# Kernel tuning notes

Measured on AMD Instinct MI355X. Metric: run time of the kernel, lower is better.

Reference implementation:

```python
import jax, jax.numpy as jnp
import numpy as np

B, DIM, H, W = 2, 128, 64, 64
DH, HEADS, K = 32, 4, 7  # dim_head, num_heads = dim // dim_head, kernel_size


def _ln(x, g, b):
    mu = jnp.mean(x, -1, keepdims=True)
    var = jnp.mean((x - mu) ** 2, -1, keepdims=True)
    return (x - mu) * jax.lax.rsqrt(var + 1e-5) * g + b


def _na2d(x, qkv_w, qkv_b, rpb, proj_w, proj_b):
    # NATTEN-style 2D neighborhood attention, dilation=1, edge-clamped windows.
    Bb, Hh, Ww, C = x.shape
    k = K
    qkv = (x @ qkv_w.T + qkv_b).reshape(Bb, Hh, Ww, 3, HEADS, DH).transpose(3, 0, 4, 1, 2, 5)
    q = qkv[0] * (DH ** -0.5)  # [B, heads, H, W, dh]
    kt, vt = qkv[1], qkv[2]
    def starts(n):
        return jnp.clip(jnp.arange(n) - k // 2, 0, n - k)
    nh = starts(Hh)[:, None] + jnp.arange(k)  # [H, k] absolute neighbor rows
    nw = starts(Ww)[:, None] + jnp.arange(k)  # [W, k] absolute neighbor cols
    ih = nh[:, None, :, None]  # [H,1,k,1]
    iw = nw[None, :, None, :]  # [1,W,1,k]
    Kw = kt[:, :, ih, iw, :]   # [B, heads, H, W, k, k, dh]
    Vw = vt[:, :, ih, iw, :]
    attn = jnp.einsum('bnhwd,bnhwijd->bnhwij', q, Kw)  # [B,heads,H,W,k,k]
    # relative positional bias, indices in [0, 2k-2]
    bih = (nh - jnp.arange(Hh)[:, None] + (k - 1))[:, None, :, None]
    biw = (nw - jnp.arange(Ww)[:, None] + (k - 1))[None, :, None, :]
    attn = attn + rpb[:, bih, biw][None]
    attn = jax.nn.softmax(attn.reshape(Bb, HEADS, Hh, Ww, k * k), -1).reshape(Bb, HEADS, Hh, Ww, k, k)
    out = jnp.einsum('bnhwij,bnhwijd->bnhwd', attn, Vw)
    out = out.transpose(0, 2, 3, 1, 4).reshape(Bb, Hh, Ww, C)
    return out @ proj_w.T + proj_b


def setup_inputs() -> dict:
    key = jax.random.key(0)
    ks = jax.random.split(key, 8)
    d = DIM
    w = lambda k_, sh: jax.random.normal(k_, sh, jnp.float32) * 0.02
    inp = {'x': jax.random.normal(ks[0], (B, DIM, H, W), jnp.float32)}
    inp.update(g1=jnp.ones(d), be1=jnp.zeros(d), g2=jnp.ones(d), be2=jnp.zeros(d),
               g3=jnp.ones(d), be3=jnp.zeros(d), g4=jnp.ones(d), be4=jnp.zeros(d))
    inp['qkv_w'] = w(ks[1], (3 * d, d)); inp['qkv_b'] = jnp.zeros(3 * d)
    inp['rpb'] = w(ks[2], (HEADS, 2 * K - 1, 2 * K - 1))
    inp['proj_w'] = w(ks[3], (d, d)); inp['proj_b'] = jnp.zeros(d)
    inp['w1'] = w(ks[4], (d, d)); inp['bl1'] = jnp.zeros(d)
    inp['w2'] = w(ks[5], (d, d)); inp['bl2'] = jnp.zeros(d)
    inp['w3'] = w(ks[6], (d, d)); inp['bl3'] = jnp.zeros(d)
    return inp


def reference(x, g1, be1, g2, be2, g3, be3, g4, be4, qkv_w, qkv_b, rpb, proj_w, proj_b, w1, bl1, w2, bl2, w3, bl3):
    x = x.transpose(0, 2, 3, 1)  # NCHW -> NHWC
    r = x
    y = _ln(x, g1, be1)
    y = _na2d(y, qkv_w, qkv_b, rpb, proj_w, proj_b)
    y = _ln(y, g2, be2)
    y = y @ w1.T + bl1
    x = y + r
    r = x
    y = _ln(x, g3, be3)
    y = y @ w2.T + bl2
    y = jax.nn.relu(y)
    y = _ln(y, g4, be4)
    y = y @ w3.T + bl3
    x = y + r
    return x.transpose(0, 3, 1, 2)  # NHWC -> NCHW
```

## Files before the change

### kernel.cpp

```cpp
#include <hip/hip_runtime.h>
#include <hip/hip_bf16.h>
#include <cstdint>

typedef short bf16x8 __attribute__((ext_vector_type(8)));
typedef float f32x4 __attribute__((ext_vector_type(4)));

#define NTOK 8192
#define QSCALE 0.17677669529663687f

__device__ inline float b2f(short s) {
  return __uint_as_float(((unsigned)(unsigned short)s) << 16);
}
__device__ inline short f2bs(float x) {
  __hip_bfloat16 b = __float2bfloat16(x);
  return *reinterpret_cast<short*>(&b);
}
__device__ inline bf16x8 ld8(const short* p) {
  short4 lo = *reinterpret_cast<const short4*>(p);
  short4 hi = *reinterpret_cast<const short4*>(p + 4);
  bf16x8 r;
  r[0] = lo.x; r[1] = lo.y; r[2] = lo.z; r[3] = lo.w;
  r[4] = hi.x; r[5] = hi.y; r[6] = hi.z; r[7] = hi.w;
  return r;
}
__device__ inline bf16x8 cvt8(float4 a, float4 c) {
  bf16x8 r;
  r[0] = f2bs(a.x); r[1] = f2bs(a.y); r[2] = f2bs(a.z); r[3] = f2bs(a.w);
  r[4] = f2bs(c.x); r[5] = f2bs(c.y); r[6] = f2bs(c.z); r[7] = f2bs(c.w);
  return r;
}

__global__ __launch_bounds__(512) void k_qkvcw(
    const float* __restrict__ x, const float* __restrict__ g,
    const float* __restrict__ be, const float* __restrict__ qkv_b,
    const float* __restrict__ qkv_w, const float* __restrict__ pw,
    const float* __restrict__ w1f, const float* __restrict__ w2f,
    const float* __restrict__ w3f, __hip_bfloat16* __restrict__ wb,
    float* __restrict__ r, __hip_bfloat16* __restrict__ qkvb) {
  __shared__ float xt[128][33];
  __shared__ __hip_bfloat16 at[32][136];
  int t = threadIdx.x;
  if (t < 256) {
    int ci = blockIdx.x * 256 + t;
    float cv;
    if (ci < 16384) cv = pw[ci];
    else if (ci < 32768) cv = w1f[ci - 16384];
    else if (ci < 49152) cv = w2f[ci - 32768];
    else cv = w3f[ci - 49152];
    wb[ci] = __float2bfloat16(cv);
  }
  int m0 = blockIdx.x * 32;
  int b = m0 >> 12;
  int p0 = m0 & 4095;
  const float* xb = x + (size_t)b * 524288;
  int tw = t & 31, th = t >> 5;
#pragma unroll
  for (int i = 0; i < 8; ++i) {
    int c = i * 16 + th;
    xt[c][tw] = xb[c * 4096 + p0 + tw];
  }
  __syncthreads();
  int wid = t >> 6, lane = t & 63;
  float gg0 = g[lane], gg1 = g[lane + 64];
  float bb0 = be[lane], bb1 = be[lane + 64];
#pragma unroll
  for (int it = 0; it < 4; ++it) {
    int tt = wid * 4 + it;
    float v0 = xt[lane][tt], v1 = xt[lane + 64][tt];
    float s = v0 + v1, sq = v0 * v0 + v1 * v1;
#pragma unroll
    for (int off = 32; off; off >>= 1) {
      s += __shfl_xor(s, off);
      sq += __shfl_xor(sq, off);
    }
    float mu = s * (1.f / 128.f);
    float var = sq * (1.f / 128.f) - mu * mu;
    float rs = rsqrtf(var + 1e-5f);
    r[(size_t)(m0 + tt) * 128 + lane] = v0;
    r[(size_t)(m0 + tt) * 128 + 64 + lane] = v1;
    at[tt][lane] = __float2bfloat16((v0 - mu) * rs * gg0 + bb0);
    at[tt][lane + 64] = __float2bfloat16((v1 - mu) * rs * gg1 + bb1);
  }
  __syncthreads();
  int mw = wid >> 2, nwq = wid & 3;
  int lr = lane & 15, kg = lane >> 4;
  bf16x8 af[4];
#pragma unroll
  for (int ks = 0; ks < 4; ++ks)
    af[ks] = *reinterpret_cast<const bf16x8*>(&at[mw * 16 + lr][ks * 32 + kg * 8]);
  f32x4 acc[6];
#pragma unroll
  for (int nf = 0; nf < 6; ++nf) acc[nf] = f32x4{0, 0, 0, 0};
#pragma unroll
  for (int nf = 0; nf < 6; ++nf) {
    int o = nwq * 96 + nf * 16 + lr;
    const float* wp = qkv_w + o * 128 + kg * 8;
#pragma unroll
    for (int ks = 0; ks < 4; ++ks) {
      float4 wa = *reinterpret_cast<const float4*>(wp + ks * 32);
      float4 wc = *reinterpret_cast<const float4*>(wp + ks * 32 + 4);
      acc[nf] = __builtin_amdgcn_mfma_f32_16x16x32_bf16(af[ks], cvt8(wa, wc),
                                                        acc[nf], 0, 0, 0);
    }
  }
#pragma unroll
  for (int nf = 0; nf < 6; ++nf) {
    int o = nwq * 96 + nf * 16 + lr;
    float bv = qkv_b[o];
    float qs = (o < 128) ? QSCALE : 1.f;
#pragma unroll
    for (int rr = 0; rr < 4; ++rr) {
      int m = m0 + mw * 16 + kg * 4 + rr;
      qkvb[(size_t)m * 384 + o] = __float2bfloat16((acc[nf][rr] + bv) * qs);
    }
  }
}

#define NB 98
#define VP 108
#define VPD 54
#define PP 132
__global__ __launch_bounds__(256) void k_attn4(
    const __hip_bfloat16* __restrict__ qkv, const float* __restrict__ rpb,
    __hip_bfloat16* __restrict__ ao) {
  __shared__ __align__(16) short smem[128 * VP + 4 * 8 * PP];
  short* Vt = smem;
  short* Pl = smem + 128 * VP;
  const short* qs = (const short*)qkv;
  int tid = threadIdx.x;
  int bid = blockIdx.x;
  int swz = (bid & 7) * 128 + (bid >> 3);
  int m0 = swz * 8;
  int b = m0 >> 12, hq = (m0 >> 6) & 63, c0 = m0 & 63;
  int hs = min(max(hq - 3, 0), 57);
  int cs0 = min(max(c0 - 3, 0), 50);
  unsigned* VtD = (unsigned*)Vt;
  {
    int g2 = tid >> 6, rp = tid & 63;
    if (rp < 49) {
      int r0 = rp * 2, r1 = r0 + 1;
      int rh0 = r0 / 14, rc0 = r0 - rh0 * 14;
      int rh1 = r1 / 14, rc1 = r1 - rh1 * 14;
      int tr0 = b * 4096 + (hs + rh0) * 64 + min(cs0 + rc0, 63);
      int tr1 = b * 4096 + (hs + rh1) * 64 + min(cs0 + rc1, 63);
#pragma unroll
      for (int gg = 0; gg < 4; ++gg) {
        int d0 = (g2 * 4 + gg) * 8;
        const short* p0 = qs + (size_t)tr0 * 384 + 256 + d0;
        const short* p1 = qs + (size_t)tr1 * 384 + 256 + d0;
        short4 a0 = *(const short4*)p0, a1 = *(const short4*)(p0 + 4);
        short4 c0v = *(const short4*)p1, c1 = *(const short4*)(p1 + 4);
        unsigned bse = (unsigned)d0 * VPD + rp;
        VtD[bse + 0 * VPD] = (unsigned short)a0.x | ((unsigned)(unsigned short)c0v.x << 16);
        VtD[bse + 1 * VPD] = (unsigned short)a0.y | ((unsigned)(unsigned short)c0v.y << 16);
        VtD[bse + 2 * VPD] = (unsigned short)a0.z | ((unsigned)(unsigned short)c0v.z << 16);
        VtD[bse + 3 * VPD] = (unsigned short)a0.w | ((unsigned)(unsigned short)c0v.w << 16);
        VtD[bse + 4 * VPD] = (unsigned short)a1.x | ((unsigned)(unsigned short)c1.x << 16);
        VtD[bse + 5 * VPD] = (unsigned short)a1.y | ((unsigned)(unsigned short)c1.y << 16);
        VtD[bse + 6 * VPD] = (unsigned short)a1.z | ((unsigned)(unsigned short)c1.z << 16);
        VtD[bse + 7 * VPD] = (unsigned short)a1.w | ((unsigned)(unsigned short)c1.w << 16);
      }
    }
  }
  for (int i = tid; i < 128 * 5; i += 256) {
    int d = i / 5, j = i - d * 5;
    VtD[d * VPD + 49 + j] = 0;
  }
  int h = tid >> 6, lane = tid & 63;
  int lr = lane & 15, kg = lane >> 4;
  int qrow = min(m0 + lr, NTOK - 1);
  bf16x8 aq = *reinterpret_cast<const bf16x8*>(qs + (size_t)qrow * 384 + h * 32 + kg * 8);
  f32x4 sc[7];
#pragma unroll
  for (int nt = 0; nt < 7; ++nt) {
    int nbr = nt * 16 + lr;
    int rw = min(nbr, NB - 1);
    int rh = rw / 14, rc = rw - rh * 14;
    int tn = b * 4096 + (hs + rh) * 64 + min(cs0 + rc, 63);
    bf16x8 bk = *reinterpret_cast<const bf16x8*>(qs + (size_t)tn * 384 + 128 + h * 32 + kg * 8);
    sc[nt] = __builtin_amdgcn_mfma_f32_16x16x32_bf16(aq, bk, f32x4{0, 0, 0, 0}, 0, 0, 0);
  }
  int offv[4], cmt[4];
#pragma unroll
  for (int rr = 0; rr < 4; ++rr) {
    int ct = c0 + kg * 4 + rr;
    int ws0 = min(max(ct - 3, 0), 57);
    offv[rr] = ws0 - cs0;
    cmt[rr] = cs0 + 6 - ct;
  }
  float mx[4] = {-3e38f, -3e38f, -3e38f, -3e38f};
#pragma unroll
  for (int nt = 0; nt < 7; ++nt) {
    int nbr = nt * 16 + lr;
    int rh = nbr / 14, rc = nbr - rh * 14;
    bool vn = nbr < NB;
    int ribase = h * 169 + (hs - hq + 6 + rh) * 13 + rc;
#pragma unroll
    for (int rr = 0; rr < 4; ++rr) {
      float v = -1e30f;
      if (vn && (unsigned)(rc - offv[rr]) < 7u) v = sc[nt][rr] + rpb[ribase + cmt[rr]];
      sc[nt][rr] = v;
      mx[rr] = fmaxf(mx[rr], v);
    }
  }
#pragma unroll
  for (int rr = 0; rr < 4; ++rr) {
    mx[rr] = fmaxf(mx[rr], __shfl_xor(mx[rr], 1));
    mx[rr] = fmaxf(mx[rr], __shfl_xor(mx[rr], 2));
    mx[rr] = fmaxf(mx[rr], __shfl_xor(mx[rr], 4));
    mx[rr] = fmaxf(mx[rr], __shfl_xor(mx[rr], 8));
  }
  float sum[4] = {0.f, 0.f, 0.f, 0.f};
#pragma unroll
  for (int nt = 0; nt < 7; ++nt)
#pragma unroll
    for (int rr = 0; rr < 4; ++rr) {
      float e = __expf(sc[nt][rr] - mx[rr]);
      sc[nt][rr] = e;
      sum[rr] += e;
    }
#pragma unroll
  for (int rr = 0; rr < 4; ++rr) {
    sum[rr] += __shfl_xor(sum[rr], 1);
    sum[rr] += __shfl_xor(sum[rr], 2);
    sum[rr] += __shfl_xor(sum[rr], 4);
    sum[rr] += __shfl_xor(sum[rr], 8);
  }
  short* Ph = Pl + h * 8 * PP;
  if (kg < 2) {
#pragma unroll
    for (int rr = 0; rr < 4; ++rr) {
      float inv = 1.f / sum[rr];
      int tok = kg * 4 + rr;
#pragma unroll
      for (int nt = 0; nt < 7; ++nt)
        Ph[tok * PP + nt * 16 + lr] = f2bs(sc[nt][rr] * inv);
      Ph[tok * PP + 112 + lr] = 0;
      Ph[tok * PP + 128 + (lr & 3)] = 0;
    }
  }
  __syncthreads();
  f32x4 o[2] = {f32x4{0, 0, 0, 0}, f32x4{0, 0, 0, 0}};
#pragma unroll
  for (int kt = 0; kt < 4; ++kt) {
    bf16x8 ap = ld8(Ph + (lr & 7) * PP + kt * 32 + kg * 8);
#pragma unroll
    for (int dt = 0; dt < 2; ++dt) {
      bf16x8 bv = ld8(Vt + (h * 32 + dt * 16 + lr) * VP + kt * 32 + kg * 8);
      o[dt] = __builtin_amdgcn_mfma_f32_16x16x32_bf16(ap, bv, o[dt], 0, 0, 0);
    }
  }
  if (kg < 2) {
#pragma unroll
    for (int dt = 0; dt < 2; ++dt)
#pragma unroll
      for (int rr = 0; rr < 4; ++rr) {
        int tok = kg * 4 + rr;
        ao[(size_t)(m0 + tok) * 128 + h * 32 + dt * 16 + lr] =
            __float2bfloat16(o[dt][rr]);
      }
  }
}

__global__ __launch_bounds__(512) void k_tail(
    const __hip_bfloat16* __restrict__ ao, const float* __restrict__ r,
    const __hip_bfloat16* __restrict__ wb, const float* __restrict__ bproj,
    const float* __restrict__ g2, const float* __restrict__ be2,
    const float* __restrict__ b1,
    const float* __restrict__ g3, const float* __restrict__ be3,
    const float* __restrict__ b2,
    const float* __restrict__ g4, const float* __restrict__ be4,
    const float* __restrict__ b3, float* __restrict__ out) {
  __shared__ __hip_bfloat16 abuf[32][136];
  __shared__ float2 red[2][4][16];
  int t = threadIdx.x, wid = t >> 6, lane = t & 63;
  int mw = wid >> 2, nwq = wid & 3;
  int lr = lane & 15, kg = lane >> 4;
  int m0 = blockIdx.x * 32;
  const __hip_bfloat16* wproj = wb;
  const __hip_bfloat16* w1 = wb + 16384;
  const __hip_bfloat16* w2 = wb + 32768;
  const __hip_bfloat16* w3 = wb + 49152;
  f32x4 acc[2];
  float x2f[2][4];

  auto gemm_glob = [&](const __hip_bfloat16* Aglob, const __hip_bfloat16* W) {
    bf16x8 af[4];
#pragma unroll
    for (int ks = 0; ks < 4; ++ks)
      af[ks] = *reinterpret_cast<const bf16x8*>(Aglob + (mw * 16 + lr) * 128 + ks * 32 + kg * 8);
#pragma unroll
    for (int nf = 0; nf < 2; ++nf) {
      int o = nwq * 32 + nf * 16 + lr;
      const __hip_bfloat16* wp = W + o * 128 + kg * 8;
      acc[nf] = f32x4{0, 0, 0, 0};
#pragma unroll
      for (int ks = 0; ks < 4; ++ks) {
        bf16x8 bfr = *reinterpret_cast<const bf16x8*>(wp + ks * 32);
        acc[nf] = __builtin_amdgcn_mfma_f32_16x16x32_bf16(af[ks], bfr, acc[nf], 0, 0, 0);
      }
    }
  };
  auto gemm_lds = [&](const __hip_bfloat16* W) {
    bf16x8 af[4];
#pragma unroll
    for (int ks = 0; ks < 4; ++ks)
      af[ks] = *reinterpret_cast<const bf16x8*>(&abuf[mw * 16 + lr][ks * 32 + kg * 8]);
#pragma unroll
    for (int nf = 0; nf < 2; ++nf) {
      int o = nwq * 32 + nf * 16 + lr;
      const __hip_bfloat16* wp = W + o * 128 + kg * 8;
      acc[nf] = f32x4{0, 0, 0, 0};
#pragma unroll
      for (int ks = 0; ks < 4; ++ks) {
        bf16x8 bfr = *reinterpret_cast<const bf16x8*>(wp + ks * 32);
        acc[nf] = __builtin_amdgcn_mfma_f32_16x16x32_bf16(af[ks], bfr, acc[nf], 0, 0, 0);
      }
    }
  };
  auto ln_store = [&](const float* g, const float* be) {
    float ps[4] = {0.f, 0.f, 0.f, 0.f}, pq[4] = {0.f, 0.f, 0.f, 0.f};
#pragma unroll
    for (int nf = 0; nf < 2; ++nf)
#pragma unroll
      for (int rr = 0; rr < 4; ++rr) {
        float v = acc[nf][rr];
        ps[rr] += v;
        pq[rr] += v * v;
      }
#pragma unroll
    for (int rr = 0; rr < 4; ++rr)
#pragma unroll
      for (int off = 1; off < 16; off <<= 1) {
        ps[rr] += __shfl_xor(ps[rr], off);
        pq[rr] += __shfl_xor(pq[rr], off);
      }
    if (lr == 0)
#pragma unroll
      for (int rr = 0; rr < 4; ++rr)
        red[mw][nwq][kg * 4 + rr] = make_float2(ps[rr], pq[rr]);
    __syncthreads();
    float mu[4], rs[4];
#pragma unroll
    for (int rr = 0; rr < 4; ++rr) {
      int r16 = kg * 4 + rr;
      float2 a0 = red[mw][0][r16], a1 = red[mw][1][r16];
      float2 a2 = red[mw][2][r16], a3 = red[mw][3][r16];
      float ssum = a0.x + a1.x + a2.x + a3.x;
      float qsum = a0.y + a1.y + a2.y + a3.y;
      mu[rr] = ssum * (1.f / 128.f);
      float var = qsum * (1.f / 128.f) - mu[rr] * mu[rr];
      rs[rr] = rsqrtf(var + 1e-5f);
    }
#pragma unroll
    for (int nf = 0; nf < 2; ++nf) {
      int o = nwq * 32 + nf * 16 + lr;
      float gv = g[o], bev = be[o];
#pragma unroll
      for (int rr = 0; rr < 4; ++rr)
        abuf[mw * 16 + kg * 4 + rr][o] =
            __float2bfloat16((acc[nf][rr] - mu[rr]) * rs[rr] * gv + bev);
    }
    __syncthreads();
  };

  gemm_glob(ao + (size_t)m0 * 128, wproj);
#pragma unroll
  for (int nf = 0; nf < 2; ++nf) {
    float bv = bproj[nwq * 32 + nf * 16 + lr];
#pragma unroll
    for (int rr = 0; rr < 4; ++rr) acc[nf][rr] += bv;
  }
  ln_store(g2, be2);

  gemm_lds(w1);
  __syncthreads();
#pragma unroll
  for (int nf = 0; nf < 2; ++nf) {
    int o = nwq * 32 + nf * 16 + lr;
    float bv = b1[o];
#pragma unroll
    for (int rr = 0; rr < 4; ++rr) {
      int m = m0 + mw * 16 + kg * 4 + rr;
      float v = acc[nf][rr] + bv + r[(size_t)m * 128 + o];
      x2f[nf][rr] = v;
      acc[nf][rr] = v;
    }
  }
  ln_store(g3, be3);

  gemm_lds(w2);
  __syncthreads();
#pragma unroll
  for (int nf = 0; nf < 2; ++nf) {
    float bv = b2[nwq * 32 + nf * 16 + lr];
#pragma unroll
    for (int rr = 0; rr < 4; ++rr) acc[nf][rr] = fmaxf(acc[nf][rr] + bv, 0.f);
  }
  ln_store(g4, be4);

  gemm_lds(w3);
#pragma unroll
  for (int nf = 0; nf < 2; ++nf) {
    int o = nwq * 32 + nf * 16 + lr;
    float bv = b3[o];
#pragma unroll
    for (int rr = 0; rr < 4; ++rr) {
      int m = m0 + mw * 16 + kg * 4 + rr;
      float v = acc[nf][rr] + bv + x2f[nf][rr];
      int bb = m >> 12, hw = m & 4095;
      out[(size_t)bb * 524288 + o * 4096 + hw] = v;
    }
  }
}

extern "C" void kernel_launch(void* const* d_in, const int* in_sizes, int n_in,
                              void* d_out, int out_size, void* d_ws,
                              size_t ws_size, hipStream_t stream) {
  const float* x = (const float*)d_in[0];
  const float* g1 = (const float*)d_in[1];
  const float* be1 = (const float*)d_in[2];
  const float* g2 = (const float*)d_in[3];
  const float* be2 = (const float*)d_in[4];
  const float* g3 = (const float*)d_in[5];
  const float* be3 = (const float*)d_in[6];
  const float* g4 = (const float*)d_in[7];
  const float* be4 = (const float*)d_in[8];
  const float* qkv_w = (const float*)d_in[9];
  const float* qkv_b = (const float*)d_in[10];
  const float* rpb = (const float*)d_in[11];
  const float* proj_w = (const float*)d_in[12];
  const float* proj_b = (const float*)d_in[13];
  const float* w1 = (const float*)d_in[14];
  const float* bl1 = (const float*)d_in[15];
  const float* w2 = (const float*)d_in[16];
  const float* bl2 = (const float*)d_in[17];
  const float* w3 = (const float*)d_in[18];
  const float* bl3 = (const float*)d_in[19];

  char* ws = (char*)d_ws;
  __hip_bfloat16* wb = (__hip_bfloat16*)ws;
  float* r = (float*)(ws + 262144);
  __hip_bfloat16* qkvb = (__hip_bfloat16*)(ws + 4456448);
  __hip_bfloat16* ao = (__hip_bfloat16*)(ws + 10747904);

  k_qkvcw<<<256, 512, 0, stream>>>(x, g1, be1, qkv_b, qkv_w, proj_w, w1, w2,
                                   w3, wb, r, qkvb);
  k_attn4<<<1024, 256, 0, stream>>>(qkvb, rpb, ao);
  k_tail<<<256, 512, 0, stream>>>(ao, r, wb, proj_b, g2, be2, bl1, g3, be3,
                                  bl2, g4, be4, bl3, (float*)d_out);
}
```

Before: 50.94 us.

## Fuse neighborhood attention with projection and MLP tail into one kernel

Merges the attention kernel and the tail kernel (projection, layernorms, MLPs) into a single kernel. Each 512-thread block handles 16 tokens as two 8-token attention sub-tiles, then runs the tail GEMMs from LDS. This removes the bf16 attention-output round trip through global memory and one kernel launch. The cost is that each block now does a 16-row MFMA tail with per-wave 16-column slices, only 512 blocks, and heavier LDS use, which may reduce occupancy and tail-GEMM efficiency.

```diff
diff --git a/kernel.cpp b/kernel.cpp
--- a/kernel.cpp
+++ b/kernel.cpp
@@ -120,32 +120,48 @@
 #define VP 108
 #define VPD 54
 #define PP 132
-__global__ __launch_bounds__(256) void k_attn4(
-    const __hip_bfloat16* __restrict__ qkv, const float* __restrict__ rpb,
-    __hip_bfloat16* __restrict__ ao) {
-  __shared__ __align__(16) short smem[128 * VP + 4 * 8 * PP];
-  short* Vt = smem;
-  short* Pl = smem + 128 * VP;
-  const short* qs = (const short*)qkv;
+#define VTSH 13824
+__global__ __launch_bounds__(512, 4) void k_fuse3(
+    const __hip_bfloat16* __restrict__ qkvb, const float* __restrict__ rpb,
+    const float* __restrict__ r, const __hip_bfloat16* __restrict__ wb,
+    const float* __restrict__ bproj,
+    const float* __restrict__ g2, const float* __restrict__ be2,
+    const float* __restrict__ b1,
+    const float* __restrict__ g3, const float* __restrict__ be3,
+    const float* __restrict__ b2,
+    const float* __restrict__ g4, const float* __restrict__ be4,
+    const float* __restrict__ b3, float* __restrict__ out) {
+  __shared__ __align__(16) short smem[2 * VTSH + 2 * 4 * 8 * PP];
+  __shared__ __align__(16) __hip_bfloat16 abuf[16][136];
+  __shared__ float2 red[8][16];
+  const short* qs = (const short*)qkvb;
   int tid = threadIdx.x;
   int bid = blockIdx.x;
-  int swz = (bid & 7) * 128 + (bid >> 3);
-  int m0 = swz * 8;
-  int b = m0 >> 12, hq = (m0 >> 6) & 63, c0 = m0 & 63;
+  int swz = (bid & 7) * 64 + (bid >> 3);
+  int m0 = swz * 16;
+  int b = m0 >> 12, hq = (m0 >> 6) & 63;
   int hs = min(max(hq - 3, 0), 57);
-  int cs0 = min(max(c0 - 3, 0), 50);
-  unsigned* VtD = (unsigned*)Vt;
-  {
-    int g2 = tid >> 6, rp = tid & 63;
+  const __hip_bfloat16* wproj = wb;
+  const __hip_bfloat16* w1 = wb + 16384;
+  const __hip_bfloat16* w2 = wb + 32768;
+  const __hip_bfloat16* w3 = wb + 49152;
+
+  {
+    int half = tid >> 8;
+    int tl = tid & 255;
+    int c0h = (m0 & 63) + half * 8;
+    int csh = min(max(c0h - 3, 0), 50);
+    unsigned* VtD = (unsigned*)(smem + half * VTSH);
+    int g2i = tl >> 6, rp = tl & 63;
     if (rp < 49) {
       int r0 = rp * 2, r1 = r0 + 1;
       int rh0 = r0 / 14, rc0 = r0 - rh0 * 14;
       int rh1 = r1 / 14, rc1 = r1 - rh1 * 14;
-      int tr0 = b * 4096 + (hs + rh0) * 64 + min(cs0 + rc0, 63);
-      int tr1 = b * 4096 + (hs + rh1) * 64 + min(cs0 + rc1, 63);
+      int tr0 = b * 4096 + (hs + rh0) * 64 + min(csh + rc0, 63);
+      int tr1 = b * 4096 + (hs + rh1) * 64 + min(csh + rc1, 63);
 #pragma unroll
       for (int gg = 0; gg < 4; ++gg) {
-        int d0 = (g2 * 4 + gg) * 8;
+        int d0 = (g2i * 4 + gg) * 8;
         const short* p0 = qs + (size_t)tr0 * 384 + 256 + d0;
         const short* p1 = qs + (size_t)tr1 * 384 + 256 + d0;
         short4 a0 = *(const short4*)p0, a1 = *(const short4*)(p0 + 4);
@@ -161,14 +177,19 @@
         VtD[bse + 7 * VPD] = (unsigned short)a1.w | ((unsigned)(unsigned short)c1.w << 16);
       }
     }
-  }
-  for (int i = tid; i < 128 * 5; i += 256) {
-    int d = i / 5, j = i - d * 5;
-    VtD[d * VPD + 49 + j] = 0;
-  }
-  int h = tid >> 6, lane = tid & 63;
+    for (int i = tl; i < 128 * 5; i += 256) {
+      int d = i / 5, j = i - d * 5;
+      VtD[d * VPD + 49 + j] = 0;
+    }
+  }
+
+  int wid = tid >> 6, lane = tid & 63;
+  int sst = wid >> 2, h = wid & 3;
   int lr = lane & 15, kg = lane >> 4;
-  int qrow = min(m0 + lr, NTOK - 1);
+  int m0s = m0 + sst * 8;
+  int c0s = (m0 & 63) + sst * 8;
+  int cs0 = min(max(c0s - 3, 0), 50);
+  int qrow = min(m0s + lr, NTOK - 1);
   bf16x8 aq = *reinterpret_cast<const bf16x8*>(qs + (size_t)qrow * 384 + h * 32 + kg * 8);
   f32x4 sc[7];
 #pragma unroll
@@ -183,7 +204,7 @@
   int offv[4], cmt[4];
 #pragma unroll
   for (int rr = 0; rr < 4; ++rr) {
-    int ct = c0 + kg * 4 + rr;
+    int ct = c0s + kg * 4 + rr;
     int ws0 = min(max(ct - 3, 0), 57);
     offv[rr] = ws0 - cs0;
     cmt[rr] = cs0 + 6 - ct;
@@ -226,7 +247,7 @@
     sum[rr] += __shfl_xor(sum[rr], 4);
     sum[rr] += __shfl_xor(sum[rr], 8);
   }
-  short* Ph = Pl + h * 8 * PP;
+  short* Ph = smem + 2 * VTSH + ((sst * 4 + h) * 8) * PP;
   if (kg < 2) {
 #pragma unroll
     for (int rr = 0; rr < 4; ++rr) {
@@ -240,94 +261,53 @@
     }
   }
   __syncthreads();
-  f32x4 o[2] = {f32x4{0, 0, 0, 0}, f32x4{0, 0, 0, 0}};
-#pragma unroll
-  for (int kt = 0; kt < 4; ++kt) {
-    bf16x8 ap = ld8(Ph + (lr & 7) * PP + kt * 32 + kg * 8);
-#pragma unroll
-    for (int dt = 0; dt < 2; ++dt) {
-      bf16x8 bv = ld8(Vt + (h * 32 + dt * 16 + lr) * VP + kt * 32 + kg * 8);
-      o[dt] = __builtin_amdgcn_mfma_f32_16x16x32_bf16(ap, bv, o[dt], 0, 0, 0);
-    }
-  }
-  if (kg < 2) {
-#pragma unroll
-    for (int dt = 0; dt < 2; ++dt)
-#pragma unroll
-      for (int rr = 0; rr < 4; ++rr) {
-        int tok = kg * 4 + rr;
-        ao[(size_t)(m0 + tok) * 128 + h * 32 + dt * 16 + lr] =
-            __float2bfloat16(o[dt][rr]);
+  {
+    const short* Vts = smem + sst * VTSH;
+    f32x4 o2[2] = {f32x4{0, 0, 0, 0}, f32x4{0, 0, 0, 0}};
+#pragma unroll
+    for (int kt = 0; kt < 4; ++kt) {
+      bf16x8 ap = ld8(Ph + (lr & 7) * PP + kt * 32 + kg * 8);
+#pragma unroll
+      for (int dt = 0; dt < 2; ++dt) {
+        bf16x8 bv = ld8(Vts + (h * 32 + dt * 16 + lr) * VP + kt * 32 + kg * 8);
+        o2[dt] = __builtin_amdgcn_mfma_f32_16x16x32_bf16(ap, bv, o2[dt], 0, 0, 0);
       }
-  }
-}
-
-__global__ __launch_bounds__(512) void k_tail(
-    const __hip_bfloat16* __restrict__ ao, const float* __restrict__ r,
-    const __hip_bfloat16* __restrict__ wb, const float* __restrict__ bproj,
-    const float* __restrict__ g2, const float* __restrict__ be2,
-    const float* __restrict__ b1,
-    const float* __restrict__ g3, const float* __restrict__ be3,
-    const float* __restrict__ b2,
-    const float* __restrict__ g4, const float* __restrict__ be4,
-    const float* __restrict__ b3, float* __restrict__ out) {
-  __shared__ __hip_bfloat16 abuf[32][136];
-  __shared__ float2 red[2][4][16];
-  int t = threadIdx.x, wid = t >> 6, lane = t & 63;
-  int mw = wid >> 2, nwq = wid & 3;
-  int lr = lane & 15, kg = lane >> 4;
-  int m0 = blockIdx.x * 32;
-  const __hip_bfloat16* wproj = wb;
-  const __hip_bfloat16* w1 = wb + 16384;
-  const __hip_bfloat16* w2 = wb + 32768;
-  const __hip_bfloat16* w3 = wb + 49152;
-  f32x4 acc[2];
-  float x2f[2][4];
-
-  auto gemm_glob = [&](const __hip_bfloat16* Aglob, const __hip_bfloat16* W) {
-    bf16x8 af[4];
-#pragma unroll
-    for (int ks = 0; ks < 4; ++ks)
-      af[ks] = *reinterpret_cast<const bf16x8*>(Aglob + (mw * 16 + lr) * 128 + ks * 32 + kg * 8);
-#pragma unroll
-    for (int nf = 0; nf < 2; ++nf) {
-      int o = nwq * 32 + nf * 16 + lr;
-      const __hip_bfloat16* wp = W + o * 128 + kg * 8;
-      acc[nf] = f32x4{0, 0, 0, 0};
-#pragma unroll
-      for (int ks = 0; ks < 4; ++ks) {
-        bf16x8 bfr = *reinterpret_cast<const bf16x8*>(wp + ks * 32);
-        acc[nf] = __builtin_amdgcn_mfma_f32_16x16x32_bf16(af[ks], bfr, acc[nf], 0, 0, 0);
-      }
-    }
-  };
+    }
+    if (kg < 2) {
+#pragma unroll
+      for (int dt = 0; dt < 2; ++dt)
+#pragma unroll
+        for (int rr = 0; rr < 4; ++rr)
+          abuf[sst * 8 + kg * 4 + rr][h * 32 + dt * 16 + lr] =
+              __float2bfloat16(o2[dt][rr]);
+    }
+  }
+  __syncthreads();
+
+  f32x4 acc;
+  float x2f[4];
+
   auto gemm_lds = [&](const __hip_bfloat16* W) {
     bf16x8 af[4];
 #pragma unroll
     for (int ks = 0; ks < 4; ++ks)
-      af[ks] = *reinterpret_cast<const bf16x8*>(&abuf[mw * 16 + lr][ks * 32 + kg * 8]);
-#pragma unroll
-    for (int nf = 0; nf < 2; ++nf) {
-      int o = nwq * 32 + nf * 16 + lr;
-      const __hip_bfloat16* wp = W + o * 128 + kg * 8;
-      acc[nf] = f32x4{0, 0, 0, 0};
-#pragma unroll
-      for (int ks = 0; ks < 4; ++ks) {
-        bf16x8 bfr = *reinterpret_cast<const bf16x8*>(wp + ks * 32);
-        acc[nf] = __builtin_amdgcn_mfma_f32_16x16x32_bf16(af[ks], bfr, acc[nf], 0, 0, 0);
-      }
+      af[ks] = *reinterpret_cast<const bf16x8*>(&abuf[lr][ks * 32 + kg * 8]);
+    int o = wid * 16 + lr;
+    const __hip_bfloat16* wp = W + o * 128 + kg * 8;
+    acc = f32x4{0, 0, 0, 0};
+#pragma unroll
+    for (int ks = 0; ks < 4; ++ks) {
+      bf16x8 bfr = *reinterpret_cast<const bf16x8*>(wp + ks * 32);
+      acc = __builtin_amdgcn_mfma_f32_16x16x32_bf16(af[ks], bfr, acc, 0, 0, 0);
     }
   };
   auto ln_store = [&](const float* g, const float* be) {
-    float ps[4] = {0.f, 0.f, 0.f, 0.f}, pq[4] = {0.f, 0.f, 0.f, 0.f};
-#pragma unroll
-    for (int nf = 0; nf < 2; ++nf)
-#pragma unroll
-      for (int rr = 0; rr < 4; ++rr) {
-        float v = acc[nf][rr];
-        ps[rr] += v;
-        pq[rr] += v * v;
-      }
+    float ps[4], pq[4];
+#pragma unroll
+    for (int rr = 0; rr < 4; ++rr) {
+      ps[rr] = acc[rr];
+      pq[rr] = acc[rr] * acc[rr];
+    }
 #pragma unroll
     for (int rr = 0; rr < 4; ++rr)
 #pragma unroll
@@ -338,76 +318,70 @@
     if (lr == 0)
 #pragma unroll
       for (int rr = 0; rr < 4; ++rr)
-        red[mw][nwq][kg * 4 + rr] = make_float2(ps[rr], pq[rr]);
+        red[wid][kg * 4 + rr] = make_float2(ps[rr], pq[rr]);
     __syncthreads();
     float mu[4], rs[4];
 #pragma unroll
     for (int rr = 0; rr < 4; ++rr) {
       int r16 = kg * 4 + rr;
-      float2 a0 = red[mw][0][r16], a1 = red[mw][1][r16];
-      float2 a2 = red[mw][2][r16], a3 = red[mw][3][r16];
-      float ssum = a0.x + a1.x + a2.x + a3.x;
-      float qsum = a0.y + a1.y + a2.y + a3.y;
+      float ssum = 0.f, qsum = 0.f;
+#pragma unroll
+      for (int w = 0; w < 8; ++w) {
+        float2 a = red[w][r16];
+        ssum += a.x;
+        qsum += a.y;
+      }
       mu[rr] = ssum * (1.f / 128.f);
       float var = qsum * (1.f / 128.f) - mu[rr] * mu[rr];
       rs[rr] = rsqrtf(var + 1e-5f);
     }
-#pragma unroll
-    for (int nf = 0; nf < 2; ++nf) {
-      int o = nwq * 32 + nf * 16 + lr;
-      float gv = g[o], bev = be[o];
-#pragma unroll
-      for (int rr = 0; rr < 4; ++rr)
-        abuf[mw * 16 + kg * 4 + rr][o] =
-            __float2bfloat16((acc[nf][rr] - mu[rr]) * rs[rr] * gv + bev);
-    }
+    int o = wid * 16 + lr;
+    float gv = g[o], bev = be[o];
+#pragma unroll
+    for (int rr = 0; rr < 4; ++rr)
+      abuf[kg * 4 + rr][o] =
+          __float2bfloat16((acc[rr] - mu[rr]) * rs[rr] * gv + bev);
     __syncthreads();
   };
 
-  gemm_glob(ao + (size_t)m0 * 128, wproj);
-#pragma unroll
-  for (int nf = 0; nf < 2; ++nf) {
-    float bv = bproj[nwq * 32 + nf * 16 + lr];
-#pragma unroll
-    for (int rr = 0; rr < 4; ++rr) acc[nf][rr] += bv;
+  gemm_lds(wproj);
+  {
+    float bv = bproj[wid * 16 + lr];
+#pragma unroll
+    for (int rr = 0; rr < 4; ++rr) acc[rr] += bv;
   }
   ln_store(g2, be2);
 
   gemm_lds(w1);
-  __syncthreads();
-#pragma unroll
-  for (int nf = 0; nf < 2; ++nf) {
-    int o = nwq * 32 + nf * 16 + lr;
+  {
+    int o = wid * 16 + lr;
     float bv = b1[o];
 #pragma unroll
     for (int rr = 0; rr < 4; ++rr) {
-      int m = m0 + mw * 16 + kg * 4 + rr;
-      float v = acc[nf][rr] + bv + r[(size_t)m * 128 + o];
-      x2f[nf][rr] = v;
-      acc[nf][rr] = v;
+      int m = m0 + kg * 4 + rr;
+      float v = acc[rr] + bv + r[(size_t)m * 128 + o];
+      x2f[rr] = v;
+      acc[rr] = v;
     }
   }
   ln_store(g3, be3);
 
   gemm_lds(w2);
-  __syncthreads();
-#pragma unroll
-  for (int nf = 0; nf < 2; ++nf) {
-    float bv = b2[nwq * 32 + nf * 16 + lr];
-#pragma unroll
-    for (int rr = 0; rr < 4; ++rr) acc[nf][rr] = fmaxf(acc[nf][rr] + bv, 0.f);
+  {
+    float bv = b2[wid * 16 + lr];
+#pragma unroll
+    for (int rr = 0; rr < 4; ++rr) acc[rr] = fmaxf(acc[rr] + bv, 0.f);
   }
   ln_store(g4, be4);
 
   gemm_lds(w3);
-#pragma unroll
-  for (int nf = 0; nf < 2; ++nf) {
-    int o = nwq * 32 + nf * 16 + lr;
+  {
+    int o = wid * 16 + lr;
     float bv = b3[o];
 #pragma unroll
     for (int rr = 0; rr < 4; ++rr) {
-      int m = m0 + mw * 16 + kg * 4 + rr;
-      float v = acc[nf][rr] + bv + x2f[nf][rr];
+      int m = m0 + kg * 4 + rr;
+      float v = acc[rr] + bv + x2f[rr];
       int bb = m >> 12, hw = m & 4095;
       out[(size_t)bb * 524288 + o * 4096 + hw] = v;
     }
@@ -442,11 +416,9 @@
   __hip_bfloat16* wb = (__hip_bfloat16*)ws;
   float* r = (float*)(ws + 262144);
   __hip_bfloat16* qkvb = (__hip_bfloat16*)(ws + 4456448);
-  __hip_bfloat16* ao = (__hip_bfloat16*)(ws + 10747904);
 
   k_qkvcw<<<256, 512, 0, stream>>>(x, g1, be1, qkv_b, qkv_w, proj_w, w1, w2,
                                    w3, wb, r, qkvb);
-  k_attn4<<<1024, 256, 0, stream>>>(qkvb, rpb, ao);
-  k_tail<<<256, 512, 0, stream>>>(ao, r, wb, proj_b, g2, be2, bl1, g3, be3,
-                                  bl2, g4, be4, bl3, (float*)d_out);
-}
+  k_fuse3<<<512, 512, 0, stream>>>(qkvb, rpb, r, wb, proj_b, g2, be2, bl1, g3,
+                                   be3, bl2, g4, be4, bl3, (float*)d_out);
+}
```

Result: faster. 49.87 us (-2.1%).
